# Kernel tuning notes

Hardware: AMD Instinct MI355X
Metric: run time of the kernel (lower is better)

## Reference

```python
import jax, jax.numpy as jnp
import numpy as np

EPS = 1e-7  # K.epsilon()


def setup_inputs() -> dict:
    key = jax.random.key(0)
    k1, k2, k3, k4, k5, k6 = jax.random.split(key, 6)
    B, S, D = 128, 1024, 256
    ATT, QDIM = 128, 128
    inp = {
        "key": jax.random.normal(k1, (B, S, D), dtype=jnp.float32),
        "query": jax.random.normal(k2, (QDIM, 1), dtype=jnp.float32),
        "mask": jax.random.randint(k3, (B, S), 0, 2, dtype=jnp.int32),
        # learned params (keras 'normal' init ~ N(0, 0.05))
        "W": 0.05 * jax.random.normal(k4, (D, ATT), dtype=jnp.float32),
        "b": 0.05 * jax.random.normal(k5, (ATT,), dtype=jnp.float32),
        "W_u": 0.05 * jax.random.normal(k6, (ATT, QDIM), dtype=jnp.float32),
    }
    return inp


def reference(key, query, mask, W, b, W_u):
    # uit = tanh(key @ W + b): (B,S,ATT)
    uit = jnp.tanh(jnp.einsum("bsd,da->bsa", key, W) + b)
    # u = W_u @ query: (ATT,1)
    u = W_u @ query
    # scores: (B,S)
    ait = jnp.einsum("bsa,a->bs", uit, u[:, 0])
    ait = jnp.exp(ait)
    ait = ait * mask.astype(jnp.float32)
    ait = ait / (jnp.sum(ait, axis=1, keepdims=True) + EPS)
    # weighted sum over sequence -> (B,D); value == key
    out = jnp.einsum("bs,bsd->bd", ait, key)
    return out
```

## Files before the change

kernel.cpp:

```cpp
#include <hip/hip_runtime.h>
#include <hip/hip_bf16.h>
#include <math.h>

#define EPS_F 1e-7f

constexpr int Bn = 128, Sn = 1024, Dn = 256, ATTn = 128, QDn = 128;
constexpr int Mn = Bn * Sn;
constexpr int BM = 128;
constexpr int NBLK = Mn / BM;
constexpr int NJ = ATTn / 16;

typedef short short8 __attribute__((ext_vector_type(8)));
typedef float f32x4  __attribute__((ext_vector_type(4)));

__device__ inline void split_bf(float f, ushort& hi, ushort& lo) {
    uint fb = __float_as_uint(f);
    hi = (ushort)(fb >> 16);
    float hf = __uint_as_float(fb & 0xffff0000u);
    float lf = f - hf;
    __hip_bfloat16 lb = __float2bfloat16(lf);
    __builtin_memcpy(&lo, &lb, 2);
}

__device__ inline float tanh_fast(float x) {
    float cx = fminf(9.0f, fmaxf(-9.0f, x));
    float e = __builtin_amdgcn_exp2f(cx * 2.8853900817779268f);
    return (e - 1.0f) * __builtin_amdgcn_rcpf(e + 1.0f);
}

__device__ inline void gload_lds16(const void* g, void* lds_base) {
    __builtin_amdgcn_global_load_lds(
        (const __attribute__((address_space(1))) unsigned int*)g,
        (__attribute__((address_space(3))) unsigned int*)lds_base, 16, 0, 0);
}

#define MFMA_BF16 __builtin_amdgcn_mfma_f32_16x16x32_bf16


__global__ __launch_bounds__(256) void k_prep(
    const float* __restrict__ Wu, const float* __restrict__ q,
    float* __restrict__ u,
    const float* __restrict__ W,
    ushort* __restrict__ Bhi)
{
    if (blockIdx.x == 0) {
        __shared__ float qs[QDn];
        int t = threadIdx.x;
        if (t < QDn) qs[t] = q[t];
        __syncthreads();
        if (t < ATTn) {
            float acc = 0.f;
            #pragma unroll 8
            for (int j = 0; j < QDn; ++j) acc += Wu[t * QDn + j] * qs[j];
            u[t] = acc;
        }
        return;
    }
    int gid  = (blockIdx.x - 1) * 256 + threadIdx.x;
    int lane = gid & 63;
    int j    = (gid >> 6) & 7;
    int ks   = gid >> 9;
    int col  = j * 16 + (lane & 15);
    int kb   = ks * 32 + (lane >> 4) * 8;
    #pragma unroll
    for (int i = 0; i < 8; ++i) {
        float f = W[(size_t)(kb + i) * ATTn + col];
        __hip_bfloat16 h = __float2bfloat16(f);
        ushort hu; __builtin_memcpy(&hu, &h, 2);
        Bhi[(size_t)gid * 8 + i] = hu;
    }
}

template<int KS>
__device__ __forceinline__ void kstep(
    const float4* smem, const float* kb,
    float4 (&kv)[4][2], f32x4 (&acc)[NJ], int lane)
{
    constexpr int S = KS & 3;
    short8 ah, al;
    {
        float4 v0 = kv[S][0], v1 = kv[S][1];
        float f[8] = {v0.x, v0.y, v0.z, v0.w, v1.x, v1.y, v1.z, v1.w};
        #pragma unroll
        for (int i = 0; i < 8; ++i) {
            ushort h, l;
            split_bf(f[i], h, l);
            ah[i] = (short)h; al[i] = (short)l;
        }
    }
    if (KS + 4 < 8) {
        kv[S][0] = *(const float4*)(kb + (KS + 4) * 32);
        kv[S][1] = *(const float4*)(kb + (KS + 4) * 32 + 4);
    }
    const float4* Bh = smem + KS * 512 + lane;
    short8 bh[3];
    bh[0] = *(const short8*)(Bh);
    bh[1] = *(const short8*)(Bh + 64);
    bh[2] = *(const short8*)(Bh + 128);
    __builtin_amdgcn_s_setprio(1);
    #pragma unroll
    for (int j = 0; j < NJ; ++j) {
        const int slot = j % 3;
        short8 cbh = bh[slot];
        if (j + 3 < NJ)
            bh[slot] = *(const short8*)(Bh + (j + 3) * 64);
        acc[j] = MFMA_BF16(ah, cbh, acc[j], 0, 0, 0);
        acc[j] = MFMA_BF16(al, cbh, acc[j], 0, 0, 0);
    }
    __builtin_amdgcn_s_setprio(0);
}

__global__ __launch_bounds__(512, 4) void k_scores(
    const float*  __restrict__ key,
    const ushort* __restrict__ Bhi,
    const float*  __restrict__ bias, const float* __restrict__ u,
    const int*    __restrict__ mask,
    float* __restrict__ P, float* __restrict__ den)
{
    __shared__ float4 smem[4096];
    float*  esp   = (float*)smem;
    float4* partp = smem + 64;

    const int t    = threadIdx.x;
    const int lane = t & 63;
    const int w    = t >> 6;
    const int gb   = blockIdx.x;
    const int row0 = gb * BM;
    const int l15  = lane & 15;
    const int lg   = lane >> 4;

    const float* kb = key + (size_t)(row0 + w * 16 + l15) * Dn + lg * 8;

    f32x4 acc[NJ];
    #pragma unroll
    for (int j = 0; j < NJ; ++j) acc[j] = (f32x4){0.f, 0.f, 0.f, 0.f};

    float4 kv[4][2];
    #pragma unroll
    for (int s = 0; s < 4; ++s) {
        kv[s][0] = *(const float4*)(kb + s * 32);
        kv[s][1] = *(const float4*)(kb + s * 32 + 4);
    }

    #pragma unroll
    for (int i = 0; i < 8; ++i)
        gload_lds16(Bhi + (size_t)(i * 512 + t) * 8, smem + (i * 512 + w * 64));
    __syncthreads();

    kstep<0>(smem, kb, kv, acc, lane);
    kstep<1>(smem, kb, kv, acc, lane);
    kstep<2>(smem, kb, kv, acc, lane);
    kstep<3>(smem, kb, kv, acc, lane);
    kstep<4>(smem, kb, kv, acc, lane);
    kstep<5>(smem, kb, kv, acc, lane);
    kstep<6>(smem, kb, kv, acc, lane);
    kstep<7>(smem, kb, kv, acc, lane);
    __syncthreads();

    float s4[4] = {0.f, 0.f, 0.f, 0.f};
    #pragma unroll
    for (int j = 0; j < NJ; ++j) {
        int col = j * 16 + l15;
        float bv = bias[col], uvv = u[col];
        #pragma unroll
        for (int reg = 0; reg < 4; ++reg)
            s4[reg] += tanh_fast(acc[j][reg] + bv) * uvv;
    }
    #pragma unroll
    for (int reg = 0; reg < 4; ++reg) {
        float s = s4[reg];
        s += __shfl_xor(s, 1);
        s += __shfl_xor(s, 2);
        s += __shfl_xor(s, 4);
        s += __shfl_xor(s, 8);
        if (l15 == 0) {
            int rl = w * 16 + lg * 4 + reg;
            esp[rl] = __builtin_amdgcn_exp2f(s * 1.4426950408889634f)
                      * (float)mask[row0 + rl];
        }
    }
    __syncthreads();

    if (t < 64) {
        float v = esp[t] + esp[t + 64];
        #pragma unroll
        for (int m = 1; m < 64; m <<= 1) v += __shfl_xor(v, m);
        if (t == 0) den[gb] = v;
    }

    {
        const float4* kt = (const float4*)(key + (size_t)(row0 + w * 16) * Dn);
        float4 a2 = make_float4(0.f, 0.f, 0.f, 0.f);
        #pragma unroll 4
        for (int s2 = 0; s2 < 16; ++s2) {
            float wv   = esp[w * 16 + s2];
            float4 kvv = kt[(size_t)s2 * 64 + lane];
            a2.x += wv * kvv.x; a2.y += wv * kvv.y;
            a2.z += wv * kvv.z; a2.w += wv * kvv.w;
        }
        partp[w * 64 + lane] = a2;
    }
    __syncthreads();

    if (t < 64) {
        float4 o = partp[t];
        #pragma unroll
        for (int wv = 1; wv < 8; ++wv) {
            float4 p = partp[wv * 64 + t];
            o.x += p.x; o.y += p.y; o.z += p.z; o.w += p.w;
        }
        *(float4*)(P + (size_t)gb * Dn + t * 4) = o;
    }
}

__global__ __launch_bounds__(256) void k_final(const float* __restrict__ P,
        const float* __restrict__ den, float* __restrict__ out) {
    int b = blockIdx.x, t = threadIdx.x;
    float dtot = 0.f;
    #pragma unroll
    for (int k = 0; k < 8; ++k) dtot += den[b * 8 + k];
    float o = 0.f;
    #pragma unroll
    for (int k = 0; k < 8; ++k) o += P[(size_t)(b * 8 + k) * Dn + t];
    out[(size_t)b * Dn + t] = o / (dtot + EPS_F);
}

extern "C" void kernel_launch(void* const* d_in, const int* in_sizes, int n_in,
                              void* d_out, int out_size, void* d_ws, size_t ws_size,
                              hipStream_t stream) {
    const float* key   = (const float*)d_in[0];
    const float* query = (const float*)d_in[1];
    const int*   mask  = (const int*)d_in[2];
    const float* W     = (const float*)d_in[3];
    const float* bias  = (const float*)d_in[4];
    const float* Wu    = (const float*)d_in[5];
    float* out = (float*)d_out;

    char* ws = (char*)d_ws;
    float*  u   = (float*)(ws);
    ushort* Bhi = (ushort*)(ws + 512);
    float*  Pp  = (float*)(ws + 66048);
    float*  den = (float*)(ws + 1114624);

    hipLaunchKernelGGL(k_prep,   dim3(17),   dim3(256), 0, stream, Wu, query, u, W, Bhi);
    hipLaunchKernelGGL(k_scores, dim3(NBLK), dim3(512), 0, stream,
                       key, Bhi, bias, u, mask, Pp, den);
    hipLaunchKernelGGL(k_final,  dim3(Bn),   dim3(256), 0, stream, Pp, den, out);
}
```

Baseline: 53.55 us.

## Double-buffer key and W tiles through LDS with async global-to-LDS loads

The key rows for the score GEMM are no longer prefetched four k-steps ahead in registers. They are now staged into XOR-swizzled, double-buffered LDS tiles with global_load_lds. The bf16 W is likewise streamed in quarters into two LDS buffers instead of being loaded all at once up front. Each k-step issues the next stage's loads, then computes on the current buffers behind a sched_barrier, which aims to overlap HBM traffic with MFMA work and cut register pressure. The cost is a block-wide barrier per k-step and extra LDS reads for the A operand.

Result: faster. 51.90 us (-3.1%).

```diff
diff --git a/kernel.cpp b/kernel.cpp
--- a/kernel.cpp
+++ b/kernel.cpp
@@ -71,16 +71,42 @@
     }
 }
 
+
+__device__ __forceinline__ void stage_Bq(
+    float4* bbuf, const ushort* __restrict__ Bhi, int q, int t, int w)
+{
+    #pragma unroll
+    for (int i = 0; i < 2; ++i) {
+        int c = i * 512 + t;
+        gload_lds16(Bhi + (size_t)(q * 1024 + c) * 8, bbuf + (i * 512 + w * 64));
+    }
+}
+
+__device__ __forceinline__ void stage_A(
+    float4* abuf, const float* __restrict__ key, int row0, int ks, int t, int w)
+{
+    #pragma unroll
+    for (int i = 0; i < 2; ++i) {
+        int s   = i * 512 + t;
+        int row = s >> 3;
+        int cl  = (s & 7) ^ (row & 7);
+        const float* src = key + (size_t)(row0 + row) * Dn + ks * 32 + cl * 4;
+        gload_lds16(src, abuf + (i * 512 + w * 64));
+    }
+}
+
 template<int KS>
-__device__ __forceinline__ void kstep(
-    const float4* smem, const float* kb,
-    float4 (&kv)[4][2], f32x4 (&acc)[NJ], int lane)
-{
-    constexpr int S = KS & 3;
+__device__ __forceinline__ void compute_ks(
+    const float4* abuf, const float4* bbuf,
+    f32x4 (&acc)[NJ], int w, int lane)
+{
+    const int l15 = lane & 15, lg = lane >> 4;
+    const int r = w * 16 + l15;
+    float4 a0 = abuf[r * 8 + ((lg * 2)     ^ (r & 7))];
+    float4 a1 = abuf[r * 8 + ((lg * 2 + 1) ^ (r & 7))];
     short8 ah, al;
     {
-        float4 v0 = kv[S][0], v1 = kv[S][1];
-        float f[8] = {v0.x, v0.y, v0.z, v0.w, v1.x, v1.y, v1.z, v1.w};
+        float f[8] = {a0.x, a0.y, a0.z, a0.w, a1.x, a1.y, a1.z, a1.w};
         #pragma unroll
         for (int i = 0; i < 8; ++i) {
             ushort h, l;
@@ -88,11 +114,7 @@
             ah[i] = (short)h; al[i] = (short)l;
         }
     }
-    if (KS + 4 < 8) {
-        kv[S][0] = *(const float4*)(kb + (KS + 4) * 32);
-        kv[S][1] = *(const float4*)(kb + (KS + 4) * 32 + 4);
-    }
-    const float4* Bh = smem + KS * 512 + lane;
+    const float4* Bh = bbuf + (KS & 1) * 512 + lane;
     short8 bh[3];
     bh[0] = *(const short8*)(Bh);
     bh[1] = *(const short8*)(Bh + 64);
@@ -110,6 +132,8 @@
     __builtin_amdgcn_s_setprio(0);
 }
 
+#define PIN() __builtin_amdgcn_sched_barrier(0)
+
 __global__ __launch_bounds__(512, 4) void k_scores(
     const float*  __restrict__ key,
     const ushort* __restrict__ Bhi,
@@ -118,6 +142,10 @@
     float* __restrict__ P, float* __restrict__ den)
 {
     __shared__ float4 smem[4096];
+    float4* B0 = smem;
+    float4* B1 = smem + 1024;
+    float4* A0 = smem + 2048;
+    float4* A1 = smem + 3072;
     float*  esp   = (float*)smem;
     float4* partp = smem + 64;
 
@@ -129,32 +157,46 @@
     const int l15  = lane & 15;
     const int lg   = lane >> 4;
 
-    const float* kb = key + (size_t)(row0 + w * 16 + l15) * Dn + lg * 8;
-
     f32x4 acc[NJ];
     #pragma unroll
     for (int j = 0; j < NJ; ++j) acc[j] = (f32x4){0.f, 0.f, 0.f, 0.f};
 
-    float4 kv[4][2];
-    #pragma unroll
-    for (int s = 0; s < 4; ++s) {
-        kv[s][0] = *(const float4*)(kb + s * 32);
-        kv[s][1] = *(const float4*)(kb + s * 32 + 4);
-    }
-
-    #pragma unroll
-    for (int i = 0; i < 8; ++i)
-        gload_lds16(Bhi + (size_t)(i * 512 + t) * 8, smem + (i * 512 + w * 64));
-    __syncthreads();
-
-    kstep<0>(smem, kb, kv, acc, lane);
-    kstep<1>(smem, kb, kv, acc, lane);
-    kstep<2>(smem, kb, kv, acc, lane);
-    kstep<3>(smem, kb, kv, acc, lane);
-    kstep<4>(smem, kb, kv, acc, lane);
-    kstep<5>(smem, kb, kv, acc, lane);
-    kstep<6>(smem, kb, kv, acc, lane);
-    kstep<7>(smem, kb, kv, acc, lane);
+    stage_Bq(B0, Bhi, 0, t, w);
+    stage_A(A0, key, row0, 0, t, w);
+    __syncthreads();
+
+    stage_Bq(B1, Bhi, 1, t, w);
+    stage_A(A1, key, row0, 1, t, w);
+    PIN();
+    compute_ks<0>(A0, B0, acc, w, lane);
+    __syncthreads();
+    stage_A(A0, key, row0, 2, t, w);
+    PIN();
+    compute_ks<1>(A1, B0, acc, w, lane);
+    __syncthreads();
+    stage_Bq(B0, Bhi, 2, t, w);
+    stage_A(A1, key, row0, 3, t, w);
+    PIN();
+    compute_ks<2>(A0, B1, acc, w, lane);
+    __syncthreads();
+    stage_A(A0, key, row0, 4, t, w);
+    PIN();
+    compute_ks<3>(A1, B1, acc, w, lane);
+    __syncthreads();
+    stage_Bq(B1, Bhi, 3, t, w);
+    stage_A(A1, key, row0, 5, t, w);
+    PIN();
+    compute_ks<4>(A0, B0, acc, w, lane);
+    __syncthreads();
+    stage_A(A0, key, row0, 6, t, w);
+    PIN();
+    compute_ks<5>(A1, B0, acc, w, lane);
+    __syncthreads();
+    stage_A(A1, key, row0, 7, t, w);
+    PIN();
+    compute_ks<6>(A0, B1, acc, w, lane);
+    __syncthreads();
+    compute_ks<7>(A1, B1, acc, w, lane);
     __syncthreads();
 
     float s4[4] = {0.f, 0.f, 0.f, 0.f};
```
